# Kernel optimization log

Measured on AMD Instinct MI355X. Metric: run time of the kernel, lower is better.

The kernel has to match this reference:

```python
import jax, jax.numpy as jnp
import numpy as np


def _pairwise_euclidean(features):
    # [N, N] Euclidean distances with a grad-safe sqrt at the zero diagonal.
    sq_norms = jnp.sum(features * features, axis=1)
    sq = sq_norms[:, None] + sq_norms[None, :] - 2.0 * (features @ features.T)
    sq = jnp.maximum(sq, 0.0)
    safe = jnp.where(sq > 0.0, sq, 1.0)
    return jnp.where(sq > 0.0, jnp.sqrt(safe), 0.0)


def setup_inputs() -> dict:
    key = jax.random.key(0)
    k1, k2 = jax.random.split(key)
    N, D = 8192, 512
    features = jax.random.normal(k1, (N, D), dtype=jnp.float32)
    adjacency_matrix = jax.random.uniform(k2, (N, N), dtype=jnp.float32)
    return {"features": features, "adjacency_matrix": adjacency_matrix, "num_neighbors": 8}


def reference(features, adjacency_matrix, num_neighbors):
    # Vectorized build_adj_hypergraph_glo:
    # per-row: normalize_tensor(adj[i]) + normalize_tensor(||f[i] - f||), then topk(k+1)
    N = features.shape[0]
    adj_norm = adjacency_matrix / jnp.sum(adjacency_matrix, axis=1, keepdims=True)
    eud = _pairwise_euclidean(features)
    eud_norm = eud / jnp.sum(eud, axis=1, keepdims=True)
    distances = adj_norm + eud_norm                     # [N, N]
    # torch.topk defaults to largest=True -> faithful: take the k+1 largest
    vals, idx = jax.lax.top_k(distances, num_neighbors + 1)  # [N, k+1]
    src = jnp.repeat(jnp.arange(N, dtype=jnp.int32), num_neighbors + 1)
    edge_index = jnp.stack([src, idx.reshape(-1).astype(jnp.int32)], axis=0)  # [2, N*(k+1)]
    edge_weights = vals.reshape(-1)                     # [N*(k+1)]
    return edge_index, edge_weights
```

## Files before the change

kernel.cpp:

```cpp
#include <hip/hip_runtime.h>
#include <hip/hip_bf16.h>
#include <math.h>


typedef short bf16x8 __attribute__((ext_vector_type(8)));
typedef float f32x4 __attribute__((ext_vector_type(4)));

__device__ __forceinline__ float fbar(float x) {
  asm volatile("" : "+v"(x));
  return x;
}
__device__ __forceinline__ unsigned short f2bf(float x) {
  union { float f; unsigned u; } v; v.f = x;
  unsigned r = (v.u + 0x7fffu + ((v.u >> 16) & 1u)) >> 16;
  return (unsigned short)r;
}
__device__ __forceinline__ float bf2f(unsigned short b) {
  union { unsigned u; float f; } v; v.u = ((unsigned)b) << 16; return v.f;
}
__device__ __forceinline__ void gload_lds16(const void* g, void* l) {
  __builtin_amdgcn_global_load_lds(
      (const __attribute__((address_space(1))) unsigned int*)g,
      (__attribute__((address_space(3))) unsigned int*)l, 16, 0, 0);
}

__global__ __launch_bounds__(256) void knn_cvt(const float* __restrict__ f,
                                               unsigned short* __restrict__ hi,
                                               unsigned short* __restrict__ lo,
                                               int n4) {
  int i = blockIdx.x * 256 + threadIdx.x;
  if (i >= n4) return;
  float4 v = ((const float4*)f)[i];
  ushort4 h, l;
  h.x = f2bf(v.x); l.x = f2bf(v.x - bf2f(h.x));
  h.y = f2bf(v.y); l.y = f2bf(v.y - bf2f(h.y));
  h.z = f2bf(v.z); l.z = f2bf(v.z - bf2f(h.z));
  h.w = f2bf(v.w); l.w = f2bf(v.w - bf2f(h.w));
  ((ushort4*)hi)[i] = h;
  ((ushort4*)lo)[i] = l;
}

__global__ __launch_bounds__(128) void knn_sqn_np(const float* __restrict__ f,
                                                  float* __restrict__ sqn32,
                                                  int N, int D) {
  int row = blockIdx.x;
  int t = threadIdx.x;
  __shared__ float a[512];
  __shared__ float R[4][8];
  const float* fr = f + (size_t)row * D;
  float4 v = ((const float4*)fr)[t];
  a[t * 4 + 0] = v.x * v.x;
  a[t * 4 + 1] = v.y * v.y;
  a[t * 4 + 2] = v.z * v.z;
  a[t * 4 + 3] = v.w * v.w;
  __syncthreads();
  if (t < 32) {
    int lf = t >> 3, m = t & 7;
    float s = a[lf * 128 + m];
    for (int g = 1; g < 16; ++g) s += a[lf * 128 + 8 * g + m];
    R[lf][m] = s;
  }
  __syncthreads();
  if (t == 0) {
    float L[4];
#pragma unroll
    for (int lf = 0; lf < 4; ++lf)
      L[lf] = ((R[lf][0] + R[lf][1]) + (R[lf][2] + R[lf][3])) +
              ((R[lf][4] + R[lf][5]) + (R[lf][6] + R[lf][7]));
    sqn32[row] = (L[0] + L[1]) + (L[2] + L[3]);
  }
}

#define TBM 128
#define TBN 128
#define TBK 32
__global__ __launch_bounds__(256) void knn_gemm_mfma(
    const unsigned short* __restrict__ fhi, const unsigned short* __restrict__ flo,
    const float* __restrict__ sqn32, unsigned short* __restrict__ eud,
    float* __restrict__ leaf, int N, int D) {
  __shared__ __align__(16) char smem[40960];

  int tid = threadIdx.x;

  int NT = N / TBM;
  int b = blockIdx.x;
  int by = 0, rem = NT;
  while (b >= rem) { b -= rem; ++by; --rem; }
  int bx = by + b;

  int i0 = by * TBM, j0 = bx * TBN;
  int wid = tid >> 6, l = tid & 63;
  int wr = wid >> 1, wc = wid & 1;
  int lr = l & 15, lk = l >> 4;

  f32x4 acc[4][4] = {};

  const unsigned short* gp = (wid & 1) ? flo : fhi;
  int rbase = (wid < 2) ? i0 : j0;
  unsigned short* Lp = (unsigned short*)(smem + wid * 8192);
  int lrow = l >> 2;
  int lblk = l & 3;
  int kblk = lblk ^ (lrow & 3);

  const unsigned short* A_h = (const unsigned short*)(smem);
  const unsigned short* A_l = (const unsigned short*)(smem + 8192);
  const unsigned short* B_h = (const unsigned short*)(smem + 16384);
  const unsigned short* B_l = (const unsigned short*)(smem + 24576);

  for (int k0 = 0; k0 < D; k0 += TBK) {
#pragma unroll
    for (int i = 0; i < 8; ++i) {
      int r = i * 16 + lrow;
      const unsigned short* g = gp + (size_t)(rbase + r) * D + k0 + kblk * 8;
      gload_lds16(g, Lp + (size_t)r * 32 + lblk * 8);
    }
    __syncthreads();

    bf16x8 ah[4], al_[4], bh[4], bl_[4];
#pragma unroll
    for (int fr = 0; fr < 4; ++fr) {
      int ra = wr * 64 + fr * 16 + lr;
      int rb = wc * 64 + fr * 16 + lr;
      int ka = (lk ^ (ra & 3)) * 8;
      int kb = (lk ^ (rb & 3)) * 8;
      ah[fr]  = *(const bf16x8*)(A_h + (size_t)ra * 32 + ka);
      al_[fr] = *(const bf16x8*)(A_l + (size_t)ra * 32 + ka);
      bh[fr]  = *(const bf16x8*)(B_h + (size_t)rb * 32 + kb);
      bl_[fr] = *(const bf16x8*)(B_l + (size_t)rb * 32 + kb);
    }
#pragma unroll
    for (int fr = 0; fr < 4; ++fr)
#pragma unroll
      for (int fc = 0; fc < 4; ++fc) {
        acc[fr][fc] = __builtin_amdgcn_mfma_f32_16x16x32_bf16(
            ah[fr], bh[fc], acc[fr][fc], 0, 0, 0);
        acc[fr][fc] = __builtin_amdgcn_mfma_f32_16x16x32_bf16(
            ah[fr], bl_[fc], acc[fr][fc], 0, 0, 0);
        acc[fr][fc] = __builtin_amdgcn_mfma_f32_16x16x32_bf16(
            al_[fr], bh[fc], acc[fr][fc], 0, 0, 0);
      }
    __syncthreads();
  }

  float (*Et)[132] = (float(*)[132])(smem);
  float (*R2)[8]   = (float(*)[8])(smem + 33792);
  float (*R3)[8]   = (float(*)[8])(smem + 35840);

  float sj[4];
#pragma unroll
  for (int fc = 0; fc < 4; ++fc) sj[fc] = sqn32[j0 + wc * 64 + fc * 16 + lr];

  bool mir = (bx != by);

#pragma unroll
  for (int pass = 0; pass < 2; ++pass) {
    if (wr == pass) {
#pragma unroll
      for (int fr = 0; fr < 4; ++fr) {
#pragma unroll
        for (int v = 0; v < 4; ++v) {
          int irow = fr * 16 + lk * 4 + v;
          int i = i0 + pass * 64 + irow;
          float si = sqn32[i];
#pragma unroll
          for (int fc = 0; fc < 4; ++fc) {
            int jcol = wc * 64 + fc * 16 + lr;
            int j = j0 + jcol;
            float sq = si + sj[fc] - 2.0f * acc[fr][fc][v];
            float e = (sq > 0.0f && i != j) ? sqrtf(sq) : 0.0f;
            Et[irow][jcol] = e;
            int q = (int)(e * 1024.0f + 0.5f);
            if (q > 65535) q = 65535;
            eud[(size_t)i * N + j] = (unsigned short)q;
          }
        }
      }
    }
    __syncthreads();

#pragma unroll
    for (int u0 = 0; u0 < 2; ++u0) {
      int u = tid + u0 * 256;
      int row = u >> 3, m = u & 7;
      float s = Et[row][m];
#pragma unroll
      for (int g = 1; g < 16; ++g) s += Et[row][8 * g + m];
      R2[row][m] = s;
    }

    if (mir) {
#pragma unroll
      for (int u0 = 0; u0 < 4; ++u0) {
        int u = tid + u0 * 256;
        int jofs = u >> 3, m = u & 7;
        float s = (pass == 0) ? 0.0f : R3[jofs][m];
#pragma unroll
        for (int g = 0; g < 8; ++g) s += Et[8 * g + m][jofs];
        R3[jofs][m] = s;
      }
      {
        int j = tid >> 1, h = tid & 1;
        size_t base = (size_t)(j0 + j) * N + i0 + pass * 64 + h * 32;
        unsigned short buf[32];
#pragma unroll
        for (int ii = 0; ii < 32; ++ii) {
          float e = Et[h * 32 + ii][j];
          int q = (int)(e * 1024.0f + 0.5f);
          if (q > 65535) q = 65535;
          buf[ii] = (unsigned short)q;
        }
#pragma unroll
        for (int q4 = 0; q4 < 4; ++q4)
          *(uint4*)(eud + base + q4 * 8) = *(uint4*)&buf[q4 * 8];
      }
    }
    __syncthreads();

    if (tid < 64) {
      float v = ((R2[tid][0] + R2[tid][1]) + (R2[tid][2] + R2[tid][3])) +
                ((R2[tid][4] + R2[tid][5]) + (R2[tid][6] + R2[tid][7]));
      leaf[(size_t)(i0 + pass * 64 + tid) * 64 + bx] = v;
    }
    if (mir && pass == 1 && tid < 128) {
      float v = ((R3[tid][0] + R3[tid][1]) + (R3[tid][2] + R3[tid][3])) +
                ((R3[tid][4] + R3[tid][5]) + (R3[tid][6] + R3[tid][7]));
      leaf[(size_t)(j0 + tid) * 64 + by] = v;
    }
    __syncthreads();
  }
}

#define CAP 640
__global__ __launch_bounds__(256) void knn_rowsel(
    const float* __restrict__ adj, const unsigned short* __restrict__ eud,
    const float* __restrict__ leaf, int* __restrict__ cand,
    float* __restrict__ cansc,
    float* __restrict__ SaOut, float* __restrict__ SeOut, int N) {
  __shared__ float arow[8192];
  __shared__ float R[64][8];
  __shared__ float Lf[64];
  __shared__ float bc[2];
  __shared__ int   cnt;
  __shared__ float ls[CAP];
  __shared__ int   lj[CAP];

  int row = blockIdx.x;
  int t = threadIdx.x;
  const float* ar = adj + (size_t)row * N;

#pragma unroll
  for (int c = 0; c < 8; ++c)
    ((float4*)arow)[c * 256 + t] = ((const float4*)ar)[c * 256 + t];
  if (t == 0) cnt = 0;
  __syncthreads();

  for (int u = t; u < 512; u += 256) {
    int lf = u >> 3, m = u & 7;
    float s = arow[lf * 128 + m];
    for (int g = 1; g < 16; ++g) s += arow[lf * 128 + 8 * g + m];
    R[lf][m] = s;
  }
  __syncthreads();
  if (t < 64)
    Lf[t] = ((R[t][0] + R[t][1]) + (R[t][2] + R[t][3])) +
            ((R[t][4] + R[t][5]) + (R[t][6] + R[t][7]));
  __syncthreads();
  for (int w = 32; w >= 1; w >>= 1) {
    if (t < w) Lf[t] = Lf[2 * t] + Lf[2 * t + 1];
    __syncthreads();
  }
  if (t == 0) { float Sa = Lf[0]; SaOut[row] = Sa; bc[0] = 1.0f / Sa; }
  __syncthreads();

  if (t < 64) Lf[t] = leaf[(size_t)row * 64 + t];
  __syncthreads();
  for (int w = 32; w >= 1; w >>= 1) {
    if (t < w) Lf[t] = Lf[2 * t] + Lf[2 * t + 1];
    __syncthreads();
  }
  if (t == 0) {
    float Se = Lf[0]; SeOut[row] = Se;
    bc[1] = (float)(1.0 / ((double)Se * 1024.0));
  }
  __syncthreads();
  float ra = bc[0], re = bc[1];

  const unsigned short* er = eud + (size_t)row * N;

#define SCORE(avc, evc) (fbar((avc) * ra) + fbar((float)(evc) * re))

  float* maxv = &R[0][0];
  float mx = -3.0e38f;
#pragma unroll
  for (int it = 0; it < 8; ++it) {
    int j = it * 1024 + t * 4;
    float4 av = *(const float4*)(arow + j);
    ushort4 ev = *(const ushort4*)(er + j);
    mx = fmaxf(mx, SCORE(av.x, ev.x));
    mx = fmaxf(mx, SCORE(av.y, ev.y));
    mx = fmaxf(mx, SCORE(av.z, ev.z));
    mx = fmaxf(mx, SCORE(av.w, ev.w));
  }
  maxv[t] = mx;
  __syncthreads();

  float tau = -3.0e38f;
  {
    int lane = t & 63;
    float a0 = maxv[lane], a1 = maxv[lane + 64];
    float a2 = maxv[lane + 128], a3 = maxv[lane + 192];
#pragma unroll
    for (int r = 0; r < 16; ++r) {
      float cv = fmaxf(fmaxf(a0, a1), fmaxf(a2, a3));
      for (int off = 32; off; off >>= 1) cv = fmaxf(cv, __shfl_xor(cv, off));
      tau = cv;
      if (a0 == cv) a0 = -3.0e38f;
      if (a1 == cv) a1 = -3.0e38f;
      if (a2 == cv) a2 = -3.0e38f;
      if (a3 == cv) a3 = -3.0e38f;
    }
  }
  __syncthreads();

#pragma unroll
  for (int it = 0; it < 8; ++it) {
    int j = it * 1024 + t * 4;
    float4 av = *(const float4*)(arow + j);
    ushort4 ev = *(const ushort4*)(er + j);
    float s0 = SCORE(av.x, ev.x);
    float s1 = SCORE(av.y, ev.y);
    float s2 = SCORE(av.z, ev.z);
    float s3 = SCORE(av.w, ev.w);
    if (s0 >= tau) { int p = atomicAdd(&cnt, 1); if (p < CAP) { ls[p] = s0; lj[p] = j + 0; } }
    if (s1 >= tau) { int p = atomicAdd(&cnt, 1); if (p < CAP) { ls[p] = s1; lj[p] = j + 1; } }
    if (s2 >= tau) { int p = atomicAdd(&cnt, 1); if (p < CAP) { ls[p] = s2; lj[p] = j + 2; } }
    if (s3 >= tau) { int p = atomicAdd(&cnt, 1); if (p < CAP) { ls[p] = s3; lj[p] = j + 3; } }
  }
#undef SCORE
  __syncthreads();
  int C = cnt < CAP ? cnt : CAP;

  if (t < 64) {
    cand[(size_t)row * 64 + t] = (t < 16) ? t : (0x40000000 + t);
    cansc[(size_t)row * 64 + t] = -3.0e38f;
  }
  __syncthreads();

  for (int i = t; i < C; i += 256) {
    float si = ls[i]; int ji = lj[i];
    int rank = 0;
    for (int k = 0; k < C; ++k) {
      float vk = ls[k]; int jk = lj[k];
      if (vk > si || (vk == si && jk < ji)) ++rank;
    }
    if (rank < 16) {
      cand[(size_t)row * 64 + rank] = ji;
      cansc[(size_t)row * 64 + rank] = si;
    }
  }
}

__global__ __launch_bounds__(256) void knn_refine(
    const float* __restrict__ f, const float* __restrict__ adj,
    const float* __restrict__ Sa, const float* __restrict__ Se,
    const int* __restrict__ cand, const float* __restrict__ cansc,
    float* __restrict__ out, int N, int D, int KP1) {
  int row = blockIdx.x;
  int t = threadIdx.x;
  int wave = t >> 6, lane = t & 63;

  __shared__ float fis[4][136];
  __shared__ float fjs[4][2][4][136];
  __shared__ float sval[64];
  __shared__ float asc[64];
  __shared__ int   ajx[64];
  __shared__ int   gidx[16];

  if (t < 64) {
    ajx[t] = cand[(size_t)row * 64 + t];
    asc[t] = cansc[(size_t)row * 64 + t];
    sval[t] = -3.0e38f;
  }
  if (t >= 64 && t < 80) gidx[t - 64] = 0;
  if (t < 128) {
    int e0 = t * 4;
    *(float4*)&fis[e0 >> 7][e0 & 127] =
        ((const float4*)(f + (size_t)row * D))[t];
  }
  __syncthreads();

  if (t < 64) {
    int myj = ajx[t]; float mys = asc[t];
    int rank = 0;
    for (int c = 0; c < 64; ++c) {
      float v = asc[c]; int jc = ajx[c];
      if (v > mys || (v == mys && jc < myj)) ++rank;
    }
    if (rank < 16) gidx[rank] = t;
  }
  __syncthreads();

  float sa = Sa[row], se = Se[row];
  int h = lane >> 5;
  int hl = lane & 31;
  int lf = hl >> 3, m = hl & 7;

#pragma unroll
  for (int p = 0; p < 2; ++p) {
    int slot = wave * 4 + p * 2 + h;
    int c = gidx[slot];
    int j = ajx[c];

    const float4* fj4 = (const float4*)(f + (size_t)j * D);
#pragma unroll
    for (int q = 0; q < 4; ++q) {
      int e0 = (hl * 4 + q) * 4;
      *(float4*)&fjs[wave][h][e0 >> 7][e0 & 127] = fj4[hl * 4 + q];
    }

    const float* ai = fis[lf];
    const float* bi = fjs[wave][h][lf];
    float d0 = ai[m] - bi[m];
    float acc = fbar(d0 * d0);
#pragma unroll
    for (int g = 1; g < 16; ++g) {
      float d = ai[8 * g + m] - bi[8 * g + m];
      acc = acc + fbar(d * d);
    }
    float u = acc + __shfl_xor(acc, 1);
    u = u + __shfl_xor(u, 2);
    u = u + __shfl_xor(u, 4);
    float s1 = u + __shfl_xor(u, 8);
    float sq = s1 + __shfl_xor(s1, 16);

    if (hl == 0) {
      float e = sq > 0.0f ? (float)sqrt((double)sq) : 0.0f;
      sval[c] = adj[(size_t)row * N + j] / sa + e / se;
    }
  }
  __syncthreads();

  if (wave == 0) {
    float v = sval[lane];
    int j = ajx[lane];
    size_t NK = (size_t)N * KP1;
    size_t ob = (size_t)row * KP1;
    for (int r = 0; r < KP1; ++r) {
      float cv = v; int cj = j;
      for (int off = 32; off; off >>= 1) {
        float ov = __shfl_xor(cv, off);
        int oj = __shfl_xor(cj, off);
        if (ov > cv || (ov == cv && oj < cj)) { cv = ov; cj = oj; }
      }
      if (lane == 0) {
        out[ob + r]          = (float)row;
        out[NK + ob + r]     = (float)cj;
        out[2 * NK + ob + r] = cv;
      }
      if (j == cj) v = -2.0f;
    }
  }
}

static inline size_t alignup(size_t x, size_t a) { return (x + a - 1) & ~(a - 1); }

extern "C" void kernel_launch(void* const* d_in, const int* in_sizes, int n_in,
                              void* d_out, int out_size, void* d_ws, size_t ws_size,
                              hipStream_t stream) {
  const float* f   = (const float*)d_in[0];
  const float* adj = (const float*)d_in[1];

  long long nn = in_sizes[1];
  int N = (int)llround(sqrt((double)nn));
  int D = in_sizes[0] / N;
  int KP1 = out_size / (3 * N);

  char* w = (char*)d_ws;
  size_t off = 0;
  float* sqn32 = (float*)(w + off); off = alignup(off + (size_t)N * 4, 256);
  float* Sa    = (float*)(w + off); off = alignup(off + (size_t)N * 4, 256);
  float* Se    = (float*)(w + off); off = alignup(off + (size_t)N * 4, 256);
  float* leaf  = (float*)(w + off); off = alignup(off + (size_t)N * 64 * 4, 256);
  int* cand    = (int*)(w + off);   off = alignup(off + (size_t)N * 64 * 4, 256);
  float* cansc = (float*)(w + off); off = alignup(off + (size_t)N * 64 * 4, 256);
  unsigned short* fhi = (unsigned short*)(w + off); off = alignup(off + (size_t)N * D * 2, 256);
  unsigned short* flo = (unsigned short*)(w + off); off = alignup(off + (size_t)N * D * 2, 256);
  unsigned short* eud = (unsigned short*)(w + off); off += (size_t)N * N * 2;
  (void)ws_size;

  int n4 = N * D / 4;
  int NT = N / TBM;
  int nblk = NT * (NT + 1) / 2;
  knn_cvt<<<(n4 + 255) / 256, 256, 0, stream>>>(f, fhi, flo, n4);
  knn_sqn_np<<<N, 128, 0, stream>>>(f, sqn32, N, D);
  knn_gemm_mfma<<<nblk, 256, 0, stream>>>(fhi, flo, sqn32, eud, leaf, N, D);
  knn_rowsel<<<N, 256, 0, stream>>>(adj, eud, leaf, cand, cansc, Sa, Se, N);
  knn_refine<<<N, 256, 0, stream>>>(f, adj, Sa, Se, cand, cansc,
                                    (float*)d_out, N, D, KP1);
}
```

Measured before the change: 399.4 us.

## Double-buffer LDS tiles in the split-bf16 distance GEMM

```diff
diff --git a/kernel.cpp b/kernel.cpp
--- a/kernel.cpp
+++ b/kernel.cpp
@@ -78,7 +78,7 @@
     const unsigned short* __restrict__ fhi, const unsigned short* __restrict__ flo,
     const float* __restrict__ sqn32, unsigned short* __restrict__ eud,
     float* __restrict__ leaf, int N, int D) {
-  __shared__ __align__(16) char smem[40960];
+  __shared__ __align__(16) char smem[65536];
 
   int tid = threadIdx.x;
 
@@ -97,24 +97,40 @@
 
   const unsigned short* gp = (wid & 1) ? flo : fhi;
   int rbase = (wid < 2) ? i0 : j0;
-  unsigned short* Lp = (unsigned short*)(smem + wid * 8192);
   int lrow = l >> 2;
   int lblk = l & 3;
   int kblk = lblk ^ (lrow & 3);
 
-  const unsigned short* A_h = (const unsigned short*)(smem);
-  const unsigned short* A_l = (const unsigned short*)(smem + 8192);
-  const unsigned short* B_h = (const unsigned short*)(smem + 16384);
-  const unsigned short* B_l = (const unsigned short*)(smem + 24576);
-
-  for (int k0 = 0; k0 < D; k0 += TBK) {
+  {
+    unsigned short* Lp = (unsigned short*)(smem + wid * 8192);
 #pragma unroll
     for (int i = 0; i < 8; ++i) {
       int r = i * 16 + lrow;
-      const unsigned short* g = gp + (size_t)(rbase + r) * D + k0 + kblk * 8;
+      const unsigned short* g = gp + (size_t)(rbase + r) * D + kblk * 8;
       gload_lds16(g, Lp + (size_t)r * 32 + lblk * 8);
     }
+  }
+
+  int buf = 0;
+  for (int k0 = 0; k0 < D; k0 += TBK) {
     __syncthreads();
+
+    if (k0 + TBK < D) {
+      unsigned short* Lp = (unsigned short*)(smem + (buf ^ 1) * 32768 + wid * 8192);
+#pragma unroll
+      for (int i = 0; i < 8; ++i) {
+        int r = i * 16 + lrow;
+        const unsigned short* g =
+            gp + (size_t)(rbase + r) * D + (k0 + TBK) + kblk * 8;
+        gload_lds16(g, Lp + (size_t)r * 32 + lblk * 8);
+      }
+    }
+
+    const char* base = smem + buf * 32768;
+    const unsigned short* A_h = (const unsigned short*)(base);
+    const unsigned short* A_l = (const unsigned short*)(base + 8192);
+    const unsigned short* B_h = (const unsigned short*)(base + 16384);
+    const unsigned short* B_l = (const unsigned short*)(base + 24576);
 
     bf16x8 ah[4], al_[4], bh[4], bl_[4];
 #pragma unroll
@@ -139,8 +155,9 @@
         acc[fr][fc] = __builtin_amdgcn_mfma_f32_16x16x32_bf16(
             al_[fr], bh[fc], acc[fr][fc], 0, 0, 0);
       }
-    __syncthreads();
-  }
+    buf ^= 1;
+  }
+  __syncthreads();
 
   float (*Et)[132] = (float(*)[132])(smem);
   float (*R2)[8]   = (float(*)[8])(smem + 33792);
@@ -200,18 +217,18 @@
       }
       {
         int j = tid >> 1, h = tid & 1;
-        size_t base = (size_t)(j0 + j) * N + i0 + pass * 64 + h * 32;
-        unsigned short buf[32];
+        size_t base2 = (size_t)(j0 + j) * N + i0 + pass * 64 + h * 32;
+        unsigned short buf2[32];
 #pragma unroll
         for (int ii = 0; ii < 32; ++ii) {
           float e = Et[h * 32 + ii][j];
           int q = (int)(e * 1024.0f + 0.5f);
           if (q > 65535) q = 65535;
-          buf[ii] = (unsigned short)q;
+          buf2[ii] = (unsigned short)q;
         }
 #pragma unroll
         for (int q4 = 0; q4 < 4; ++q4)
-          *(uint4*)(eud + base + q4 * 8) = *(uint4*)&buf[q4 * 8];
+          *(uint4*)(eud + base2 + q4 * 8) = *(uint4*)&buf2[q4 * 8];
       }
     }
     __syncthreads();
```

Result: no change. 395.1 us (-1.1%).
